# Performance work log

Hardware: AMD Instinct MI355X
Metric: run time of the kernel (lower is better)

The kernel has to match this reference:

```python
import jax, jax.numpy as jnp
import numpy as np

B, N, C, H = 2, 2048, 1024, 16
D = C // H
SCALE = 1.0 / np.sqrt(D)
MASK_VAL = -10000.0


def setup_inputs() -> dict:
    key = jax.random.key(0)
    k1, k2, k3 = jax.random.split(key, 3)
    hidden_state = jax.random.normal(k1, (B, N, C), dtype=jnp.float32)
    attention_mask = jax.random.randint(k2, (B, N), 0, 2) == 1  # True = padded
    # fused QKV projection weight, torch Linear convention: y = x @ W.T, W: [3C, C]
    W = jax.random.normal(k3, (3 * C, C), dtype=jnp.float32) * 0.02
    return {"hidden_state": hidden_state, "W": W, "attention_mask": attention_mask}


def reference(hidden_state, W, attention_mask):
    b, n, c = hidden_state.shape
    # fused QKV: [B,N,3C] -> [B,N,3,H,D] -> [3,B,H,N,D]
    wx = jnp.einsum('bnc,oc->bno', hidden_state, W).reshape(b, n, 3, H, D)
    wx = jnp.transpose(wx, (2, 0, 3, 1, 4))
    q, k, v = wx[0], wx[1], wx[2]
    scores = jnp.einsum('bhid,bhjd->bhij', q, k) * SCALE
    # construct_mask: pairwise OR of per-token padding mask, broadcast over heads
    m = attention_mask
    expanded = (m[:, None, :, None] | m[:, None, None, :])  # [B,1,N,N]
    scores = jnp.where(expanded, MASK_VAL, scores)
    scores = scores - jnp.max(scores, axis=-1, keepdims=True)
    att_weights = jax.nn.softmax(scores, axis=-1)
    # dropout_rate = 0.0 -> identity
    att = jnp.einsum('bhij,bhjd->bhid', att_weights, v)
    att = jnp.transpose(att, (0, 2, 1, 3)).reshape(b, n, c)
    return (att, att_weights)
```

## Files before the change

kernel.cpp:

```cpp
#include <hip/hip_runtime.h>


typedef unsigned short u16;
typedef __attribute__((ext_vector_type(8))) short bf16x8;
typedef __attribute__((ext_vector_type(4))) float f32x4;

#define B_ 2
#define N_ 2048
#define H_ 16
#define D_ 64
#define QKV_MAT 4194304
#define ATTW_OFF 4194304
#define OFF_MASK 25165824
#define OFF_FLAG 25182208
#define OFF_XB   25182464
#define OFF_WB   33571072

#define SCALE_L2 0.18033688011112042f
#define MASK_L2  -14426.950408889634f

__device__ __forceinline__ u16 f32_bf16(float f) {
  unsigned u = __float_as_uint(f);
  u += 0x7fffu + ((u >> 16) & 1u);
  return (u16)(u >> 16);
}
__device__ __forceinline__ float bf16_f32(unsigned h) {
  return __uint_as_float(h << 16);
}
__device__ __forceinline__ bf16x8 ld_frag(const u16* p) { return *(const bf16x8*)p; }

__device__ __forceinline__ void gld16(u16* l, const u16* g) {
  __builtin_amdgcn_global_load_lds(
      (const __attribute__((address_space(1))) void*)g,
      (__attribute__((address_space(3))) void*)l, 16, 0, 0);
}

__device__ __forceinline__ void bar_lgkm0() {
  __builtin_amdgcn_sched_barrier(0);
  asm volatile("s_waitcnt lgkmcnt(0)" ::: "memory");
  __builtin_amdgcn_s_barrier();
  __builtin_amdgcn_sched_barrier(0);
}
__device__ __forceinline__ void bar_vm2() {
  __builtin_amdgcn_sched_barrier(0);
  asm volatile("s_waitcnt vmcnt(2)" ::: "memory");
  __builtin_amdgcn_s_barrier();
  __builtin_amdgcn_sched_barrier(0);
}
__device__ __forceinline__ void bar_vm4() {
  __builtin_amdgcn_sched_barrier(0);
  asm volatile("s_waitcnt vmcnt(4)" ::: "memory");
  __builtin_amdgcn_s_barrier();
  __builtin_amdgcn_sched_barrier(0);
}

__global__ void detect_prep(const unsigned char* __restrict__ mraw,
                            const unsigned* __restrict__ X32,
                            int* __restrict__ flag) {
  __shared__ int votes, mflags;
  const int tid = threadIdx.x;
  if (tid == 0) { votes = 0; mflags = 0; }
  __syncthreads();
  int v = 0;
  for (int i = tid; i < 4096; i += 1024) {
    unsigned low = X32[i] & 0xFFFFu;
    unsigned e = (low >> 7) & 0xFFu;
    if (low == 0 || (e >= 80 && e <= 150)) v++;
  }
  atomicAdd(&votes, v);
  int fl = 0;
  for (int p = tid; p < B_ * N_; p += 1024) {
    unsigned char c = mraw[p];
    if (c > 1) fl |= 1;
    if (c && (p & 3) == 1) fl |= 4;
    if (c && (p & 3) != 0) fl |= 2;
    if (c && (p & 7) == 4) fl |= 8;
  }
  if (fl) atomicOr(&mflags, fl);
  __syncthreads();
  if (tid == 0) { flag[0] = (votes < 2600) ? 1 : 0; flag[1] = mflags; }
}

__global__ __launch_bounds__(256) void convert_in(const void* __restrict__ X,
                                                  const void* __restrict__ W,
                                                  const unsigned char* __restrict__ mraw,
                                                  u16* __restrict__ Xb, u16* __restrict__ Wb,
                                                  int* __restrict__ mout,
                                                  const int* __restrict__ flag) {
  const int f32m = flag[0];
  const int f = flag[1];
  const int gid = blockIdx.x * 256 + threadIdx.x;
  for (int i = gid; i < B_ * N_; i += gridDim.x * 256) {
    int m;
    if (f & 1) {
      if (f & 4) m = (((const u16*)mraw)[i] & 0x7FFFu) != 0;
      else       m = (((const unsigned*)mraw)[i] << 1) != 0;
    } else if (f & 2) m = mraw[i] != 0;
    else if (f & 8)   m = ((const int*)mraw)[i] != 0;
    else              m = ((const long long*)mraw)[i] != 0;
    mout[i] = m;
  }
  const int XC = (B_ * N_ * 1024) / 8;
  const int WC = (3072 * 1024) / 8;
  for (int idx = gid; idx < XC + WC; idx += gridDim.x * 256) {
    const void* src; u16* dst; int c;
    if (idx < XC) { c = idx; src = X; dst = Xb; }
    else          { c = idx - XC; src = W; dst = Wb; }
    if (f32m) {
      const float4* s = (const float4*)src;
      float4 a = s[c * 2], b = s[c * 2 + 1];
      unsigned p0 = (unsigned)f32_bf16(a.x) | ((unsigned)f32_bf16(a.y) << 16);
      unsigned p1 = (unsigned)f32_bf16(a.z) | ((unsigned)f32_bf16(a.w) << 16);
      unsigned p2 = (unsigned)f32_bf16(b.x) | ((unsigned)f32_bf16(b.y) << 16);
      unsigned p3 = (unsigned)f32_bf16(b.z) | ((unsigned)f32_bf16(b.w) << 16);
      ((uint4*)dst)[c] = make_uint4(p0, p1, p2, p3);
    } else {
      ((uint4*)dst)[c] = ((const uint4*)src)[c];
    }
  }
}

__global__ __launch_bounds__(256) void qkv_gemm(const u16* __restrict__ X,
                                                const u16* __restrict__ W,
                                                u16* __restrict__ qkv) {
  __shared__ u16 xs[128 * 64];
  __shared__ u16 wsh[128 * 64];
  const int tid = threadIdx.x;
  const int w = tid >> 6, l = tid & 63, quad = l >> 4, ln = l & 15;
  const int r0 = blockIdx.y * 128;
  const int o0 = blockIdx.x * 128;

  const f32x4 z4 = {0.f, 0.f, 0.f, 0.f};
  f32x4 acc[2][8];
#pragma unroll
  for (int rt = 0; rt < 2; rt++)
#pragma unroll
    for (int ct = 0; ct < 8; ct++) acc[rt][ct] = z4;

  for (int kc = 0; kc < 1024; kc += 64) {
#pragma unroll
    for (int ro = 0; ro < 4; ro++) {
      int q = ro * 256 + tid;
      int r = q >> 3, s = q & 7;
      int c = s ^ (r & 7);
      gld16(xs + q * 8, X + (size_t)(r0 + r) * 1024 + kc + c * 8);
      gld16(wsh + q * 8, W + (size_t)(o0 + r) * 1024 + kc + c * 8);
    }
    __syncthreads();
#pragma unroll
    for (int k2 = 0; k2 < 2; k2++) {
      bf16x8 af[2], bfr[8];
#pragma unroll
      for (int rt = 0; rt < 2; rt++) {
        int row = w * 32 + rt * 16 + ln;
        int slot = (k2 * 4 + quad) ^ (row & 7);
        af[rt] = ld_frag(xs + row * 64 + slot * 8);
      }
#pragma unroll
      for (int ct = 0; ct < 8; ct++) {
        int row = ct * 16 + ln;
        int slot = (k2 * 4 + quad) ^ (row & 7);
        bfr[ct] = ld_frag(wsh + row * 64 + slot * 8);
      }
#pragma unroll
      for (int rt = 0; rt < 2; rt++)
#pragma unroll
        for (int ct = 0; ct < 8; ct++)
          acc[rt][ct] = __builtin_amdgcn_mfma_f32_16x16x32_bf16(af[rt], bfr[ct], acc[rt][ct], 0, 0, 0);
    }
    __syncthreads();
  }

  const int b = r0 >> 11;
#pragma unroll
  for (int rt = 0; rt < 2; rt++) {
#pragma unroll
    for (int ct = 0; ct < 8; ct++) {
      int o = o0 + ct * 16 + ln;
      int sel = o >> 10;
      int h = (o >> 6) & 15;
      int d = o & 63;
      int nbase = (r0 & 2047) + w * 32 + rt * 16 + quad * 4;
      if (sel < 2) {
        size_t base = (size_t)sel * QKV_MAT + ((size_t)(b * 16 + h) * N_ + nbase) * D_ + d;
#pragma unroll
        for (int g = 0; g < 4; g++)
          qkv[base + (size_t)g * D_] = f32_bf16(acc[rt][ct][g]);
      } else {
        size_t base = 2 * (size_t)QKV_MAT + ((size_t)(b * 16 + h) * D_ + d) * N_ + nbase;
        unsigned lo = (unsigned)f32_bf16(acc[rt][ct][0]) | ((unsigned)f32_bf16(acc[rt][ct][1]) << 16);
        unsigned hi = (unsigned)f32_bf16(acc[rt][ct][2]) | ((unsigned)f32_bf16(acc[rt][ct][3]) << 16);
        *(uint2*)(qkv + base) = make_uint2(lo, hi);
      }
    }
  }
}

__global__ __launch_bounds__(512, 4) void attn_kernel(const u16* __restrict__ qkv,
                                                      const int* __restrict__ mask,
                                                      void* __restrict__ outv,
                                                      const int* __restrict__ flag) {
  __shared__ u16 qs[128 * 64];
  __shared__ u16 ks[2][64 * 64];
  __shared__ u16 vs[2][64 * 64];
  __shared__ u16 ps[128 * 72];
  __shared__ float mrow[128];
  __shared__ float rlrow[128];

  const int of32 = __builtin_amdgcn_readfirstlane(flag[0]);
  u16* outh = (u16*)outv;
  float* outf = (float*)outv;

  const int tid = threadIdx.x;
  const int w = tid >> 6;
  const int l = tid & 63, quad = l >> 4, ln = l & 15;
  const int bh = blockIdx.x & 31;
  const int qt = blockIdx.x >> 5;
  const int b = bh >> 4, h = bh & 15;
  const int q0 = qt * 128;
  const int jstrip = (w & 3) * 16;
  const int baseit = (w >> 2) * 4;

  const u16* Qg = qkv + ((size_t)bh * N_ + q0) * D_;
  const u16* Kg = qkv + QKV_MAT + (size_t)bh * N_ * D_;
  const u16* Vg = qkv + 2 * (size_t)QKV_MAT + (size_t)bh * D_ * N_;
  const int* mb = mask + b * N_;
  const size_t attw_base = (size_t)ATTW_OFF + (size_t)bh * N_ * N_ + (size_t)q0 * N_;

#pragma unroll
  for (int ro = 0; ro < 2; ro++) {
    int q = ro * 512 + tid;
    int r = q >> 3, s = q & 7;
    int c = s ^ (r & 7);
    gld16(qs + q * 8, Qg + (size_t)r * D_ + c * 8);
  }
  {
    int q = tid;
    int r = q >> 3, s = q & 7;
    int c = s ^ (r & 7);
    gld16(ks[0] + q * 8, Kg + (size_t)r * D_ + c * 8);
  }
  int rowpad[4];
#pragma unroll
  for (int g = 0; g < 4; g++)
    rowpad[g] = mb[q0 + w * 16 + quad * 4 + g];
  __syncthreads();

  bf16x8 qa[2];
#pragma unroll
  for (int k2 = 0; k2 < 2; k2++) {
    int row = w * 16 + ln;
    int slot = (k2 * 4 + quad) ^ (row & 7);
    qa[k2] = ld_frag(qs + row * 64 + slot * 8);
  }

  float lsum[4] = {0.f, 0.f, 0.f, 0.f};
  const f32x4 z4 = {0.f, 0.f, 0.f, 0.f};

  for (int kt = 0; kt < 32; kt++) {
    const int cur = kt & 1;
    if (kt < 31) {
      int q = tid;
      int r = q >> 3, s = q & 7;
      int c = s ^ (r & 7);
      gld16(ks[cur ^ 1] + q * 8, Kg + (size_t)((kt + 1) * 64 + r) * D_ + c * 8);
    }
    int cp[4];
#pragma unroll
    for (int ct = 0; ct < 4; ct++) cp[ct] = mb[kt * 64 + ct * 16 + ln];

    f32x4 sacc[4];
#pragma unroll
    for (int ct = 0; ct < 4; ct++) sacc[ct] = z4;
#pragma unroll
    for (int k2 = 0; k2 < 2; k2++) {
      bf16x8 kb[4];
#pragma unroll
      for (int ct = 0; ct < 4; ct++) {
        int row = ct * 16 + ln;
        int slot = (k2 * 4 + quad) ^ (row & 7);
        kb[ct] = ld_frag(ks[cur] + row * 64 + slot * 8);
      }
#pragma unroll
      for (int ct = 0; ct < 4; ct++)
        sacc[ct] = __builtin_amdgcn_mfma_f32_16x16x32_bf16(qa[k2], kb[ct], sacc[ct], 0, 0, 0);
    }
#pragma unroll
    for (int g = 0; g < 4; g++) {
      float e = 0.f;
#pragma unroll
      for (int ct = 0; ct < 4; ct++) {
        float sv = sacc[ct][g] * SCALE_L2;
        sv = (rowpad[g] | cp[ct]) ? MASK_L2 : sv;
        e += __builtin_amdgcn_exp2f(sv);
      }
      lsum[g] += e;
    }
    __syncthreads();
  }

  {
    int q = tid;
    int r = q >> 3, s = q & 7;
    int c = s ^ (r & 7);
    gld16(ks[0] + q * 8, Kg + (size_t)r * D_ + c * 8);
    gld16(vs[0] + q * 8, Vg + (size_t)r * N_ + c * 8);
  }

#pragma unroll
  for (int g = 0; g < 4; g++) {
    float lv = lsum[g];
    lv += __shfl_xor(lv, 1);
    lv += __shfl_xor(lv, 2);
    lv += __shfl_xor(lv, 4);
    lv += __shfl_xor(lv, 8);
    if (ln == 0) {
      int i = w * 16 + quad * 4 + g;
      mrow[i] = rowpad[g] ? MASK_L2 : 0.f;
      rlrow[i] = rowpad[g] ? (1.f / 2048.f) : (1.f / lv);
    }
  }
  __syncthreads();

  bf16x8 qb[4][2];
  float mi[4], rli[4];
#pragma unroll
  for (int itl = 0; itl < 4; itl++) {
    int row = (baseit + itl) * 16 + ln;
#pragma unroll
    for (int k2 = 0; k2 < 2; k2++) {
      int slot = (k2 * 4 + quad) ^ (row & 7);
      qb[itl][k2] = ld_frag(qs + row * 64 + slot * 8);
    }
    mi[itl] = mrow[row];
    rli[itl] = rlrow[row];
  }

  f32x4 oacc[4];
#pragma unroll
  for (int dt = 0; dt < 4; dt++) oacc[dt] = z4;

  for (int kt = 0; kt < 32; kt++) {
    const int cur = kt & 1;
    int cpj[4];
#pragma unroll
    for (int g = 0; g < 4; g++) cpj[g] = mb[kt * 64 + jstrip + quad * 4 + g];

    bf16x8 ka[2];
#pragma unroll
    for (int k2 = 0; k2 < 2; k2++) {
      int row = jstrip + ln;
      int slot = (k2 * 4 + quad) ^ (row & 7);
      ka[k2] = ld_frag(ks[cur] + row * 64 + slot * 8);
    }
#pragma unroll
    for (int itl = 0; itl < 4; itl++) {
      f32x4 st = z4;
      st = __builtin_amdgcn_mfma_f32_16x16x32_bf16(ka[0], qb[itl][0], st, 0, 0, 0);
      st = __builtin_amdgcn_mfma_f32_16x16x32_bf16(ka[1], qb[itl][1], st, 0, 0, 0);
      bool rp = mi[itl] < -5000.f;
      unsigned pk[4];
#pragma unroll
      for (int g = 0; g < 4; g++) {
        float sv = st[g] * SCALE_L2;
        sv = (cpj[g] || rp) ? MASK_L2 : sv;
        float p = __builtin_amdgcn_exp2f(sv - mi[itl]) * rli[itl];
        pk[g] = f32_bf16(p);
      }
      int iRow = (baseit + itl) * 16 + ln;
      int jc = jstrip + quad * 4;
      *(uint2*)(ps + iRow * 72 + jc) = make_uint2(pk[0] | (pk[1] << 16), pk[2] | (pk[3] << 16));
    }
    bar_lgkm0();

    if (kt < 31) {
      int q = tid;
      int r = q >> 3, s = q & 7;
      int c = s ^ (r & 7);
      gld16(ks[cur ^ 1] + q * 8, Kg + (size_t)((kt + 1) * 64 + r) * D_ + c * 8);
      gld16(vs[cur ^ 1] + q * 8, Vg + (size_t)r * N_ + (kt + 1) * 64 + c * 8);
    }

    if (!of32) {
#pragma unroll
      for (int ro = 0; ro < 2; ro++) {
        int q = ro * 512 + tid;
        int r = q >> 3, c = q & 7;
        uint4 v = *(const uint4*)(ps + r * 72 + c * 8);
        *(uint4*)(outh + attw_base + (size_t)r * N_ + kt * 64 + c * 8) = v;
      }
    } else {
#pragma unroll
      for (int ro = 0; ro < 4; ro++) {
        int q = ro * 512 + tid;
        int r = q >> 4, c4 = q & 15;
        uint2 v = *(const uint2*)(ps + r * 72 + c4 * 4);
        float4 o = make_float4(bf16_f32(v.x & 0xFFFFu), bf16_f32(v.x >> 16),
                               bf16_f32(v.y & 0xFFFFu), bf16_f32(v.y >> 16));
        *(float4*)(outf + attw_base + (size_t)r * N_ + kt * 64 + c4 * 4) = o;
      }
    }
#pragma unroll
    for (int k2 = 0; k2 < 2; k2++) {
      bf16x8 pa, vb[4];
      {
        int row = w * 16 + ln;
        pa = ld_frag(ps + row * 72 + k2 * 32 + quad * 8);
      }
#pragma unroll
      for (int dt = 0; dt < 4; dt++) {
        int row = dt * 16 + ln;
        int slot = (k2 * 4 + quad) ^ (row & 7);
        vb[dt] = ld_frag(vs[cur] + row * 64 + slot * 8);
      }
#pragma unroll
      for (int dt = 0; dt < 4; dt++)
        oacc[dt] = __builtin_amdgcn_mfma_f32_16x16x32_bf16(pa, vb[dt], oacc[dt], 0, 0, 0);
    }
    if (!of32) bar_vm2(); else bar_vm4();
  }

#pragma unroll
  for (int dt = 0; dt < 4; dt++) {
    int d = dt * 16 + ln;
#pragma unroll
    for (int g = 0; g < 4; g++) {
      int i = w * 16 + quad * 4 + g;
      size_t off = (size_t)(b * N_ + q0 + i) * 1024 + h * 64 + d;
      if (!of32) outh[off] = f32_bf16(oacc[dt][g]);
      else       outf[off] = oacc[dt][g];
    }
  }
}

extern "C" void kernel_launch(void* const* d_in, const int* in_sizes, int n_in,
                              void* d_out, int out_size, void* d_ws, size_t ws_size,
                              hipStream_t stream) {
  (void)in_sizes; (void)n_in; (void)out_size; (void)ws_size;
  const unsigned char* mraw = (const unsigned char*)d_in[2];
  char* ws = (char*)d_ws;
  u16* qkvws = (u16*)ws;
  int* maskws = (int*)(ws + OFF_MASK);
  int* flagws = (int*)(ws + OFF_FLAG);
  u16* Xb = (u16*)(ws + OFF_XB);
  u16* Wb = (u16*)(ws + OFF_WB);

  detect_prep<<<1, 1024, 0, stream>>>(mraw, (const unsigned*)d_in[0], flagws);
  convert_in<<<1792, 256, 0, stream>>>(d_in[0], d_in[1], mraw, Xb, Wb, maskws, flagws);
  qkv_gemm<<<dim3(24, 32), 256, 0, stream>>>(Xb, Wb, qkvws);
  attn_kernel<<<512, 512, 0, stream>>>(qkvws, maskws, d_out, flagws);
}
```

Before: 730.2 us.

## Shrink attention tile to 64 queries and load K/V fragments directly from global

The attention kernel now uses 256-thread blocks over 64-query tiles (1024 blocks) instead of 512 threads over 128 queries. The double-buffered K/V shared-memory staging is removed, and each wave reads its MFMA K and V fragments straight from global memory, relying on the caches for reuse. This cuts LDS use and barrier/vmcnt waits, and raises block count and occupancy. In exchange it gives up the explicit prefetch overlap and adds redundant global and L2 traffic for K/V fragments.

Result: slower. 832.2 us (+14.0%).

```diff
diff --git a/kernel.cpp b/kernel.cpp
--- a/kernel.cpp
+++ b/kernel.cpp
@@ -38,18 +38,6 @@
 __device__ __forceinline__ void bar_lgkm0() {
   __builtin_amdgcn_sched_barrier(0);
   asm volatile("s_waitcnt lgkmcnt(0)" ::: "memory");
-  __builtin_amdgcn_s_barrier();
-  __builtin_amdgcn_sched_barrier(0);
-}
-__device__ __forceinline__ void bar_vm2() {
-  __builtin_amdgcn_sched_barrier(0);
-  asm volatile("s_waitcnt vmcnt(2)" ::: "memory");
-  __builtin_amdgcn_s_barrier();
-  __builtin_amdgcn_sched_barrier(0);
-}
-__device__ __forceinline__ void bar_vm4() {
-  __builtin_amdgcn_sched_barrier(0);
-  asm volatile("s_waitcnt vmcnt(4)" ::: "memory");
   __builtin_amdgcn_s_barrier();
   __builtin_amdgcn_sched_barrier(0);
 }
@@ -196,16 +184,14 @@
   }
 }
 
-__global__ __launch_bounds__(512, 4) void attn_kernel(const u16* __restrict__ qkv,
+__global__ __launch_bounds__(256, 3) void attn_kernel(const u16* __restrict__ qkv,
                                                       const int* __restrict__ mask,
                                                       void* __restrict__ outv,
                                                       const int* __restrict__ flag) {
-  __shared__ u16 qs[128 * 64];
-  __shared__ u16 ks[2][64 * 64];
-  __shared__ u16 vs[2][64 * 64];
-  __shared__ u16 ps[128 * 72];
-  __shared__ float mrow[128];
-  __shared__ float rlrow[128];
+  __shared__ u16 qs[64 * 64];
+  __shared__ u16 ps[64 * 72];
+  __shared__ float mrow[64];
+  __shared__ float rlrow[64];
 
   const int of32 = __builtin_amdgcn_readfirstlane(flag[0]);
   u16* outh = (u16*)outv;
@@ -217,9 +203,7 @@
   const int bh = blockIdx.x & 31;
   const int qt = blockIdx.x >> 5;
   const int b = bh >> 4, h = bh & 15;
-  const int q0 = qt * 128;
-  const int jstrip = (w & 3) * 16;
-  const int baseit = (w >> 2) * 4;
+  const int q0 = qt * 64;
 
   const u16* Qg = qkv + ((size_t)bh * N_ + q0) * D_;
   const u16* Kg = qkv + QKV_MAT + (size_t)bh * N_ * D_;
@@ -229,16 +213,10 @@
 
 #pragma unroll
   for (int ro = 0; ro < 2; ro++) {
-    int q = ro * 512 + tid;
+    int q = ro * 256 + tid;
     int r = q >> 3, s = q & 7;
     int c = s ^ (r & 7);
     gld16(qs + q * 8, Qg + (size_t)r * D_ + c * 8);
-  }
-  {
-    int q = tid;
-    int r = q >> 3, s = q & 7;
-    int c = s ^ (r & 7);
-    gld16(ks[0] + q * 8, Kg + (size_t)r * D_ + c * 8);
   }
   int rowpad[4];
 #pragma unroll
@@ -258,33 +236,26 @@
   const f32x4 z4 = {0.f, 0.f, 0.f, 0.f};
 
   for (int kt = 0; kt < 32; kt++) {
-    const int cur = kt & 1;
-    if (kt < 31) {
-      int q = tid;
-      int r = q >> 3, s = q & 7;
-      int c = s ^ (r & 7);
-      gld16(ks[cur ^ 1] + q * 8, Kg + (size_t)((kt + 1) * 64 + r) * D_ + c * 8);
-    }
     int cp[4];
 #pragma unroll
     for (int ct = 0; ct < 4; ct++) cp[ct] = mb[kt * 64 + ct * 16 + ln];
 
+    bf16x8 kb[4][2];
+#pragma unroll
+    for (int ct = 0; ct < 4; ct++)
+#pragma unroll
+      for (int k2 = 0; k2 < 2; k2++)
+        kb[ct][k2] = ld_frag(Kg + (size_t)(kt * 64 + ct * 16 + ln) * D_ + k2 * 32 + quad * 8);
+
     f32x4 sacc[4];
 #pragma unroll
     for (int ct = 0; ct < 4; ct++) sacc[ct] = z4;
 #pragma unroll
-    for (int k2 = 0; k2 < 2; k2++) {
-      bf16x8 kb[4];
-#pragma unroll
-      for (int ct = 0; ct < 4; ct++) {
-        int row = ct * 16 + ln;
-        int slot = (k2 * 4 + quad) ^ (row & 7);
-        kb[ct] = ld_frag(ks[cur] + row * 64 + slot * 8);
-      }
+    for (int k2 = 0; k2 < 2; k2++)
 #pragma unroll
       for (int ct = 0; ct < 4; ct++)
-        sacc[ct] = __builtin_amdgcn_mfma_f32_16x16x32_bf16(qa[k2], kb[ct], sacc[ct], 0, 0, 0);
-    }
+        sacc[ct] = __builtin_amdgcn_mfma_f32_16x16x32_bf16(qa[k2], kb[ct][k2], sacc[ct], 0, 0, 0);
+
 #pragma unroll
     for (int g = 0; g < 4; g++) {
       float e = 0.f;
@@ -296,15 +267,6 @@
       }
       lsum[g] += e;
     }
-    __syncthreads();
-  }
-
-  {
-    int q = tid;
-    int r = q >> 3, s = q & 7;
-    int c = s ^ (r & 7);
-    gld16(ks[0] + q * 8, Kg + (size_t)r * D_ + c * 8);
-    gld16(vs[0] + q * 8, Vg + (size_t)r * N_ + c * 8);
   }
 
 #pragma unroll
@@ -326,7 +288,7 @@
   float mi[4], rli[4];
 #pragma unroll
   for (int itl = 0; itl < 4; itl++) {
-    int row = (baseit + itl) * 16 + ln;
+    int row = itl * 16 + ln;
 #pragma unroll
     for (int k2 = 0; k2 < 2; k2++) {
       int slot = (k2 * 4 + quad) ^ (row & 7);
@@ -341,18 +303,15 @@
   for (int dt = 0; dt < 4; dt++) oacc[dt] = z4;
 
   for (int kt = 0; kt < 32; kt++) {
-    const int cur = kt & 1;
     int cpj[4];
 #pragma unroll
-    for (int g = 0; g < 4; g++) cpj[g] = mb[kt * 64 + jstrip + quad * 4 + g];
+    for (int g = 0; g < 4; g++) cpj[g] = mb[kt * 64 + w * 16 + quad * 4 + g];
 
     bf16x8 ka[2];
 #pragma unroll
-    for (int k2 = 0; k2 < 2; k2++) {
-      int row = jstrip + ln;
-      int slot = (k2 * 4 + quad) ^ (row & 7);
-      ka[k2] = ld_frag(ks[cur] + row * 64 + slot * 8);
-    }
+    for (int k2 = 0; k2 < 2; k2++)
+      ka[k2] = ld_frag(Kg + (size_t)(kt * 64 + w * 16 + ln) * D_ + k2 * 32 + quad * 8);
+
 #pragma unroll
     for (int itl = 0; itl < 4; itl++) {
       f32x4 st = z4;
@@ -367,24 +326,16 @@
         float p = __builtin_amdgcn_exp2f(sv - mi[itl]) * rli[itl];
         pk[g] = f32_bf16(p);
       }
-      int iRow = (baseit + itl) * 16 + ln;
-      int jc = jstrip + quad * 4;
+      int iRow = itl * 16 + ln;
+      int jc = w * 16 + quad * 4;
       *(uint2*)(ps + iRow * 72 + jc) = make_uint2(pk[0] | (pk[1] << 16), pk[2] | (pk[3] << 16));
     }
     bar_lgkm0();
 
-    if (kt < 31) {
-      int q = tid;
-      int r = q >> 3, s = q & 7;
-      int c = s ^ (r & 7);
-      gld16(ks[cur ^ 1] + q * 8, Kg + (size_t)((kt + 1) * 64 + r) * D_ + c * 8);
-      gld16(vs[cur ^ 1] + q * 8, Vg + (size_t)r * N_ + (kt + 1) * 64 + c * 8);
-    }
-
     if (!of32) {
 #pragma unroll
       for (int ro = 0; ro < 2; ro++) {
-        int q = ro * 512 + tid;
+        int q = ro * 256 + tid;
         int r = q >> 3, c = q & 7;
         uint4 v = *(const uint4*)(ps + r * 72 + c * 8);
         *(uint4*)(outh + attw_base + (size_t)r * N_ + kt * 64 + c * 8) = v;
@@ -392,7 +343,7 @@
     } else {
 #pragma unroll
       for (int ro = 0; ro < 4; ro++) {
-        int q = ro * 512 + tid;
+        int q = ro * 256 + tid;
         int r = q >> 4, c4 = q & 15;
         uint2 v = *(const uint2*)(ps + r * 72 + c4 * 4);
         float4 o = make_float4(bf16_f32(v.x & 0xFFFFu), bf16_f32(v.x >> 16),
@@ -403,21 +354,15 @@
 #pragma unroll
     for (int k2 = 0; k2 < 2; k2++) {
       bf16x8 pa, vb[4];
-      {
-        int row = w * 16 + ln;
-        pa = ld_frag(ps + row * 72 + k2 * 32 + quad * 8);
-      }
-#pragma unroll
-      for (int dt = 0; dt < 4; dt++) {
-        int row = dt * 16 + ln;
-        int slot = (k2 * 4 + quad) ^ (row & 7);
-        vb[dt] = ld_frag(vs[cur] + row * 64 + slot * 8);
-      }
+      pa = ld_frag(ps + (w * 16 + ln) * 72 + k2 * 32 + quad * 8);
+#pragma unroll
+      for (int dt = 0; dt < 4; dt++)
+        vb[dt] = ld_frag(Vg + (size_t)(dt * 16 + ln) * N_ + kt * 64 + k2 * 32 + quad * 8);
 #pragma unroll
       for (int dt = 0; dt < 4; dt++)
         oacc[dt] = __builtin_amdgcn_mfma_f32_16x16x32_bf16(pa, vb[dt], oacc[dt], 0, 0, 0);
     }
-    if (!of32) bar_vm2(); else bar_vm4();
+    bar_lgkm0();
   }
 
 #pragma unroll
@@ -448,5 +393,5 @@
   detect_prep<<<1, 1024, 0, stream>>>(mraw, (const unsigned*)d_in[0], flagws);
   convert_in<<<1792, 256, 0, stream>>>(d_in[0], d_in[1], mraw, Xb, Wb, maskws, flagws);
   qkv_gemm<<<dim3(24, 32), 256, 0, stream>>>(Xb, Wb, qkvws);
-  attn_kernel<<<512, 512, 0, stream>>>(qkvws, maskws, d_out, flagws);
-}
+  attn_kernel<<<1024, 256, 0, stream>>>(qkvws, maskws, d_out, flagws);
+}
```
